# Performance work log

Measured on AMD Instinct MI355X. Metric: run time of the kernel, lower is better.

The kernel has to match this reference:

```python
import jax, jax.numpy as jnp
import numpy as np
from jax import lax

D = 256      # key/query dim
D_F = 256    # diff feature channels
C_TOK = 1    # leading context tokens in query_vit
EPS = 1e-6


def conv2d(x, w, b, pad):
    out = lax.conv_general_dilated(x, w, (1, 1), [(pad, pad), (pad, pad)],
                                   dimension_numbers=('NCHW', 'OIHW', 'NCHW'))
    return out + b[None, :, None, None]


def gn1(x, g, b):
    # GroupNorm with 1 group: normalize over (C,H,W) per sample
    mu = jnp.mean(x, axis=(1, 2, 3), keepdims=True)
    var = jnp.var(x, axis=(1, 2, 3), keepdims=True)
    xn = (x - mu) * lax.rsqrt(var + EPS)
    return xn * g[None, :, None, None] + b[None, :, None, None]


def resize_bilinear_ac(x, Ho, Wo):
    # F.interpolate(mode='bilinear', align_corners=True)
    B, C, H, W = x.shape
    ys = jnp.linspace(0.0, H - 1.0, Ho)
    xs = jnp.linspace(0.0, W - 1.0, Wo)
    y0 = jnp.floor(ys).astype(jnp.int32)
    y1 = jnp.minimum(y0 + 1, H - 1)
    wy = (ys - y0)[None, None, :, None]
    x0 = jnp.floor(xs).astype(jnp.int32)
    x1 = jnp.minimum(x0 + 1, W - 1)
    wx = (xs - x0)[None, None, None, :]
    r = x[:, :, y0, :] * (1.0 - wy) + x[:, :, y1, :] * wy
    return r[:, :, :, x0] * (1.0 - wx) + r[:, :, :, x1] * wx


def setup_inputs() -> dict:
    key = jax.random.key(0)
    ks = jax.random.split(key, 12)
    B, Hd, Wd, Ht, Wt = 8, 64, 64, 32, 32

    def kaiming(k, shape, fan_in):
        return jax.random.normal(k, shape, jnp.float32) * np.sqrt(2.0 / fan_in)

    return {
        'query_vit': jax.random.normal(ks[0], (B, C_TOK + Ht * Wt, D), jnp.float32),
        'feat_diff_cat': jax.random.normal(ks[1], (B, 5 * D_F, Hd, Wd), jnp.float32),
        'rb_w1': kaiming(ks[2], (D_F, 5 * D_F, 3, 3), 5 * D_F * 9), 'rb_b1': jnp.zeros((D_F,), jnp.float32),
        'rb_w2': kaiming(ks[3], (D_F, D_F, 3, 3), D_F * 9), 'rb_b2': jnp.zeros((D_F,), jnp.float32),
        'rb_ws': kaiming(ks[4], (D_F, 5 * D_F, 1, 1), 5 * D_F), 'rb_bs': jnp.zeros((D_F,), jnp.float32),
        'ln_g': jnp.ones((D_F,), jnp.float32), 'ln_b': jnp.zeros((D_F,), jnp.float32),
        'key_w': kaiming(ks[5], (D, D_F, 1, 1), D_F), 'key_b': jnp.zeros((D,), jnp.float32),
        'val_w': kaiming(ks[6], (D_F, D_F, 1, 1), D_F), 'val_b': jnp.zeros((D_F,), jnp.float32),
        'dh0_w': kaiming(ks[7], (D_F, D_F, 3, 3), D_F * 9), 'dh0_b': jnp.zeros((D_F,), jnp.float32),
        'dh1_w': kaiming(ks[8], (D_F, D_F, 3, 3), D_F * 9), 'dh1_b': jnp.zeros((D_F,), jnp.float32),
    }


def reference(query_vit, feat_diff_cat, rb_w1, rb_b1, rb_w2, rb_b2, rb_ws, rb_bs,
              ln_g, ln_b, key_w, key_b, val_w, val_b, dh0_w, dh0_b, dh1_w, dh1_b):
    B, _, h_diff, w_diff = feat_diff_cat.shape
    N = query_vit.shape[1] - C_TOK
    h_trm = w_trm = int(N ** 0.5)

    # ResBlock_ysh(D_f*5 -> D_f): conv3x3 + relu + conv3x3, 1x1-projected residual
    h = jax.nn.relu(conv2d(feat_diff_cat, rb_w1, rb_b1, 1))
    h = conv2d(h, rb_w2, rb_b2, 1)
    feat_diff = jax.nn.relu(h + conv2d(feat_diff_cat, rb_ws, rb_bs, 0))

    fln = gn1(feat_diff, ln_g, ln_b)
    key_diff = conv2d(fln, key_w, key_b, 0).reshape(B, D, -1)          # (B, D, HW)
    value_diff = conv2d(fln, val_w, val_b, 0).reshape(B, D_F, -1)      # (B, Df, HW)
    value_diff = jnp.transpose(value_diff, (0, 2, 1))                  # (B, HW, Df)

    # cross attention: (B, C+N, D) @ (B, D, HW) -> softmax -> @ (B, HW, Df)
    scores = jnp.einsum('bnd,bdm->bnm', query_vit, key_diff) * (D ** -0.5)
    attn = jax.nn.softmax(scores, axis=-1)
    out_cross = jnp.einsum('bnm,bmf->bnf', attn, value_diff)           # (B, C+N, Df)

    out_cross_c = out_cross[:, :C_TOK, :]
    out_p = jnp.transpose(out_cross[:, C_TOK:, :], (0, 2, 1)).reshape(B, D_F, h_trm, w_trm)
    out_p = jax.nn.relu(conv2d(out_p, dh0_w, dh0_b, 1))
    out_p = resize_bilinear_ac(out_p, h_diff, w_diff)
    out_p = out_p + feat_diff                                          # DropPath(0) = identity
    out_p = jax.nn.relu(conv2d(gn1(out_p, ln_g, ln_b), dh1_w, dh1_b, 1)) + out_p
    return out_cross_c, out_p
```

## Files before the change

kernel.cpp:

```cpp
#include <hip/hip_runtime.h>
#include <cstdint>
#include <cstddef>

typedef __attribute__((ext_vector_type(4))) float     f32x4;
typedef __attribute__((ext_vector_type(8))) __bf16    bf16x8;
typedef __attribute__((ext_vector_type(8))) short     short8;
typedef __attribute__((ext_vector_type(4))) unsigned short u16x4;
typedef unsigned short u16;

__device__ __forceinline__ float b2f(u16 u) {
  unsigned x = ((unsigned)u) << 16;
  float f;
  __builtin_memcpy(&f, &x, 4);
  return f;
}
__device__ __forceinline__ u16 f2b(float f) {
  unsigned u;
  __builtin_memcpy(&u, &f, 4);
  return (u16)((u + 0x7FFFu + ((u >> 16) & 1u)) >> 16);
}

struct GP {
  const u16*  A;
  const u16*  B;
  const float* bias;
  const void* aux;
  void*       C;
  float*      out0;
  float*      st;
  long long   aBS, bBS, cBS, auxBS, biasBS;
  int Ktot, Mrows, ldc;
  int cin, logW, wpad, poff;
  float scale;
};

#define GLDS16(g, l)                                                        \
  __builtin_amdgcn_global_load_lds(                                         \
      (const void __attribute__((address_space(1)))*)(g),                   \
      (void __attribute__((address_space(3)))*)(l), 16, 0, 0)

struct G256 {
  const u16* A;
  const u16* B;
  float* P;
  long long aBS;
  int Ktot, cin, logW, wpad, poff;
};

__global__ __launch_bounds__(512, 2) void k_gemm256(G256 gp) {
  const int tid = threadIdx.x;
  const int l = tid & 63, w = tid >> 6;
  const int lr = l & 15, lc = l >> 4;
  const int id = blockIdx.x;
  const int xcd = id & 7, slot = id >> 3;
  const int sp = xcd >> 2;
  const int u = (xcd & 3) * 32 + slot;
  const int mt = u & 15;
  const int b = u >> 4;
  const int m0 = mt << 8;
  const int wm = w >> 2, wn = w & 3;

  __shared__ __align__(16) u16 sm[4][16384];
  u16* smb = &sm[0][0];

  f32x4 acc[8][4];
#pragma unroll
  for (int i = 0; i < 8; ++i)
#pragma unroll
    for (int j = 0; j < 4; ++j) acc[i][j] = (f32x4){0.f, 0.f, 0.f, 0.f};

  const u16* Ab = gp.A + (size_t)b * gp.aBS;
  const u16* aS[2];
  const u16* bS[2];
#pragma unroll
  for (int j = 0; j < 2; ++j) {
    const int r = j * 128 + w * 16 + (l >> 2);
    const int p = m0 + r;
    const int y = p >> gp.logW, x = p & ((1 << gp.logW) - 1);
    const int sw = ((l & 3) ^ ((r >> 1) & 3)) << 3;
    aS[j] = Ab + (size_t)((y + gp.poff) * gp.wpad + (x + gp.poff)) * gp.cin + sw;
    bS[j] = gp.B + (size_t)r * gp.Ktot + sw;
  }

  const int NH = gp.Ktot >> 6;
  const int kt0h = sp * NH;
  int off = kt0h << 5;
  int tap = off / gp.cin;
  int kcS = off - tap * gp.cin;
  int dxS = tap % 3;
  int tapS = (tap / 3) * gp.wpad + dxS;
  int hgS = kt0h;

  auto stage = [&](int h) {
    const int hb = h & 3;
    const int kB = hgS << 5;
    const int kA = tapS * gp.cin + kcS;
    kcS += 32;
    if (kcS == gp.cin) {
      kcS = 0; ++dxS; ++tapS;
      if (dxS == 3) { dxS = 0; tapS += gp.wpad - 3; }
    }
    ++hgS;
    u16* base = smb + hb * 16384 + (w * 16) * 32 + l * 8;
    GLDS16(aS[0] + kA, base);
    GLDS16(aS[1] + kA, base + 4096);
    GLDS16(bS[0] + kB, base + 8192);
    GLDS16(bS[1] + kB, base + 12288);
  };

  stage(0);
  stage(1);
  stage(2);
  asm volatile("s_waitcnt vmcnt(8)" ::: "memory");
  __builtin_amdgcn_s_barrier();

  bf16x8 av[8], bv[4];
  {
    const char* b0 = (const char*)smb;
#pragma unroll
    for (int mi = 0; mi < 8; ++mi) {
      const int row = wm * 128 + mi * 16 + lr;
      av[mi] = *(const bf16x8*)(b0 + row * 64 + ((lc ^ ((row >> 1) & 3)) << 4));
    }
#pragma unroll
    for (int ni = 0; ni < 4; ++ni) {
      const int row = wn * 64 + ni * 16 + lr;
      bv[ni] = *(const bf16x8*)(b0 + 16384 + row * 64 +
                                ((lc ^ ((row >> 1) & 3)) << 4));
    }
  }

  for (int h = 0; h < NH; ++h) {
    if (h + 3 < NH) stage(h + 3);
    const int rem = NH - 1 - h;
    if (rem > 0) {
      if (rem > 2)
        asm volatile("s_waitcnt vmcnt(8)" ::: "memory");
      else if (rem == 2)
        asm volatile("s_waitcnt vmcnt(4)" ::: "memory");
      else
        asm volatile("s_waitcnt vmcnt(0)" ::: "memory");
      asm volatile("s_waitcnt lgkmcnt(0)" ::: "memory");
      __builtin_amdgcn_s_barrier();
    }

    const bool pf = (h + 1 < NH);
    const char* nxt = (const char*)smb + ((h + 1) & 3) * 32768;

#pragma unroll
    for (int mi = 0; mi < 8; ++mi) {
      const int row = wm * 128 + mi * 16 + lr;
      const int sw = (lc ^ ((row >> 1) & 3)) << 4;
#pragma unroll
      for (int ni = 0; ni < 4; ++ni)
        acc[mi][ni] = __builtin_amdgcn_mfma_f32_16x16x32_bf16(
            av[mi], bv[ni], acc[mi][ni], 0, 0, 0);
      if (pf) av[mi] = *(const bf16x8*)(nxt + row * 64 + sw);
    }
    if (pf) {
#pragma unroll
      for (int ni = 0; ni < 4; ++ni) {
        const int row = wn * 64 + ni * 16 + lr;
        bv[ni] = *(const bf16x8*)(nxt + 16384 + row * 64 +
                                  ((lc ^ ((row >> 1) & 3)) << 4));
      }
    }
  }

  float* P = gp.P + ((size_t)sp * 128 + b * 16 + mt) * 65536;
#pragma unroll
  for (int mi = 0; mi < 8; ++mi)
#pragma unroll
    for (int ni = 0; ni < 4; ++ni) {
      const int ncol = wn * 64 + ni * 16 + lr;
      const int mloc = wm * 128 + mi * 16 + lc * 4;
#pragma unroll
      for (int r = 0; r < 4; ++r)
        P[(size_t)(mloc + r) * 256 + ncol] = acc[mi][ni][r];
    }
}

__global__ __launch_bounds__(256) void k_reduceH1(const float* __restrict__ P,
                                                  const float* __restrict__ bias,
                                                  u16* __restrict__ o) {
  const int i4 = blockIdx.x * 256 + threadIdx.x;
  const int flat = i4 << 2;
  const int n0 = flat & 255;
  const int mloc = (flat >> 8) & 255;
  const int gm = flat >> 16;
  const f32x4 a = *(const f32x4*)(P + (size_t)gm * 65536 + mloc * 256 + n0);
  const f32x4 c = *(const f32x4*)(P + (size_t)(128 + gm) * 65536 + mloc * 256 + n0);
  const f32x4 bb = *(const f32x4*)(bias + n0);
  const int batch = gm >> 4;
  const int mg = (gm & 15) * 256 + mloc;
  const int y = mg >> 6, x = mg & 63;
  u16x4 r;
#pragma unroll
  for (int k = 0; k < 4; ++k) r[k] = f2b(fmaxf(a[k] + c[k] + bb[k], 0.f));
  *(u16x4*)(o + ((size_t)batch * 4356 + (size_t)(y + 1) * 66 + x + 1) * 256 + n0) = r;
}

template <int AMODE, int CW>
__global__ __launch_bounds__(512, 2) void k_gemm8(GP gp) {
  const int tid = threadIdx.x;
  const int l = tid & 63, w = tid >> 6;
  const int b = blockIdx.z;
  const int m0 = blockIdx.x * 128;
  const int wm = w >> 2, wn = w & 3;
  const int lr = l & 15, lc = l >> 4;

  __shared__ __align__(16) u16 sm[2][24576];

  f32x4 acc[4][4];
#pragma unroll
  for (int i = 0; i < 4; ++i)
#pragma unroll
    for (int j = 0; j < 4; ++j) acc[i][j] = (f32x4){0.f, 0.f, 0.f, 0.f};

  const u16* Ab = gp.A + (size_t)b * gp.aBS;
  const u16* Bb = gp.B + (size_t)b * gp.bBS;
  const int scoff = (((tid & 7) ^ ((tid >> 3) & 7)) << 3);

  const u16* aP[2];
  const u16* aP2[2];
#pragma unroll
  for (int i = 0; i < 2; ++i) {
    const int p = m0 + i * 64 + (tid >> 3);
    const int y = p >> 6, x = p & 63;
    aP[i] = Ab + (size_t)(y * 66 + x) * gp.cin + scoff;
    if (AMODE == 2) {
      const u16* Xb = (const u16*)gp.aux + (size_t)b * gp.auxBS;
      aP2[i] = Xb + (size_t)((y + 1) * 66 + (x + 1)) * 1280 + scoff;
    }
  }
  const u16* bP[4];
#pragma unroll
  for (int i = 0; i < 4; ++i)
    bP[i] = Bb + (size_t)(i * 64 + (tid >> 3)) * gp.Ktot + scoff;

  const int NT = gp.Ktot >> 6;
  const int seg1t = (AMODE == 2) ? 36 : 0x7fffffff;
  int kcS = 0, tapS = 0, dxS = 0, nstg = 0;

  auto stage = [&](int buf) {
    const int kt = nstg++;
    const int kB = kt << 6;
    u16* sA = &sm[buf][0] + (w << 9);
    u16* sB = &sm[buf][8192] + (w << 9);
    if (AMODE == 2 && kt >= seg1t) {
      const int kA = (kt - seg1t) << 6;
      GLDS16(aP2[0] + kA, sA);
      GLDS16(aP2[1] + kA, sA + 4096);
    } else {
      const int kA = tapS * gp.cin + kcS;
      kcS += 64;
      if (kcS == gp.cin) {
        kcS = 0; ++dxS; ++tapS;
        if (dxS == 3) { dxS = 0; tapS += 63; }
      }
      GLDS16(aP[0] + kA, sA);
      GLDS16(aP[1] + kA, sA + 4096);
    }
    GLDS16(bP[0] + kB, sB);
    GLDS16(bP[1] + kB, sB + 4096);
    GLDS16(bP[2] + kB, sB + 8192);
    GLDS16(bP[3] + kB, sB + 12288);
  };

  stage(0);
  asm volatile("s_waitcnt vmcnt(0)" ::: "memory");
  __builtin_amdgcn_s_barrier();

  for (int t = 0; t < NT; ++t) {
    const int buf = t & 1;
    const u16* sAc = &sm[buf][0];
    const u16* sBc = &sm[buf][8192];
    if (t + 1 < NT) stage(buf ^ 1);

    bf16x8 av0[4], av1[4], bv0[4], bv1[4];
#pragma unroll
    for (int mi = 0; mi < 4; ++mi) {
      const int row = wm * 64 + mi * 16 + lr;
      av0[mi] = *(const bf16x8*)(sAc + row * 64 + (((0 + lc) ^ (row & 7)) << 3));
      av1[mi] = *(const bf16x8*)(sAc + row * 64 + (((4 + lc) ^ (row & 7)) << 3));
    }
#pragma unroll
    for (int ni = 0; ni < 4; ++ni) {
      const int row = wn * 64 + ni * 16 + lr;
      bv0[ni] = *(const bf16x8*)(sBc + row * 64 + (((0 + lc) ^ (row & 7)) << 3));
      bv1[ni] = *(const bf16x8*)(sBc + row * 64 + (((4 + lc) ^ (row & 7)) << 3));
    }
#pragma unroll
    for (int mi = 0; mi < 4; ++mi)
#pragma unroll
      for (int ni = 0; ni < 4; ++ni)
        acc[mi][ni] = __builtin_amdgcn_mfma_f32_16x16x32_bf16(
            av0[mi], bv0[ni], acc[mi][ni], 0, 0, 0);
#pragma unroll
    for (int mi = 0; mi < 4; ++mi)
#pragma unroll
      for (int ni = 0; ni < 4; ++ni)
        acc[mi][ni] = __builtin_amdgcn_mfma_f32_16x16x32_bf16(
            av1[mi], bv1[ni], acc[mi][ni], 0, 0, 0);
    asm volatile("s_waitcnt vmcnt(0)" ::: "memory");
    __builtin_amdgcn_s_barrier();
  }

  float lsum = 0.f, lsq = 0.f;
#pragma unroll
  for (int mi = 0; mi < 4; ++mi) {
#pragma unroll
    for (int ni = 0; ni < 4; ++ni) {
      const int ncol = wn * 64 + ni * 16 + lr;
      const int mbase = m0 + wm * 64 + mi * 16 + lc * 4;
      const float bv_ = gp.bias[ncol];
      if constexpr (CW == 8) {
        float* F = (float*)gp.C + (size_t)b * gp.cBS;
        u16* FB = (u16*)gp.out0 + (size_t)b * gp.cBS;
#pragma unroll
        for (int r = 0; r < 4; ++r) {
          float v = fmaxf(acc[mi][ni][r] + bv_, 0.f);
          const size_t idx = (size_t)(mbase + r) * 256 + ncol;
          F[idx] = v;
          FB[idx] = f2b(v);
          lsum += v;
          lsq += v * v;
        }
      } else {
        float* Cf =
            (float*)gp.C + (size_t)b * gp.cBS + (size_t)ncol * 4096 + mbase;
        const float* mid = (const float*)gp.aux + (size_t)b * gp.auxBS;
        f32x4 o;
#pragma unroll
        for (int r = 0; r < 4; ++r) {
          float v = fmaxf(acc[mi][ni][r] + bv_, 0.f);
          o[r] = v + mid[(size_t)(mbase + r) * 256 + ncol];
        }
        *(f32x4*)Cf = o;
      }
    }
  }
  if constexpr (CW == 8) {
    __syncthreads();
#pragma unroll
    for (int o = 32; o; o >>= 1) {
      lsum += __shfl_down(lsum, o);
      lsq += __shfl_down(lsq, o);
    }
    float* red = (float*)&sm[0][0];
    if (l == 0) { red[w * 2] = lsum; red[w * 2 + 1] = lsq; }
    __syncthreads();
    if (tid == 0) {
      float s = 0.f, s2 = 0.f;
#pragma unroll
      for (int k = 0; k < 8; ++k) { s += red[k * 2]; s2 += red[k * 2 + 1]; }
      atomicAdd(&gp.st[b * 2], s);
      atomicAdd(&gp.st[b * 2 + 1], s2);
    }
  }
}

template <int AMODE, int CW, bool RELU>
__global__ __launch_bounds__(256, 2) void k_gemm(GP gp) {
  const int tid = threadIdx.x;
  const int l = tid & 63, w = tid >> 6;
  const int b = blockIdx.z;
  const int m0 = blockIdx.x * 128, n0 = blockIdx.y * 128;
  const int wm = w >> 1, wn = w & 1;

  __shared__ __align__(16) u16 smA[128 * 64];
  __shared__ __align__(16) u16 smB[128 * 64];

  f32x4 acc[4][4];
#pragma unroll
  for (int i = 0; i < 4; ++i)
#pragma unroll
    for (int j = 0; j < 4; ++j) acc[i][j] = (f32x4){0.f, 0.f, 0.f, 0.f};

  const u16* Ab = gp.A + (size_t)b * gp.aBS;
  const u16* Bb = gp.B + (size_t)b * gp.bBS;

  const int scoff = (((l & 7) ^ (l >> 3)) << 3);

  const u16* aRow[4];
  const u16* bRow[4];
  u16* ldsA[4];
  u16* ldsB[4];
#pragma unroll
  for (int i = 0; i < 4; ++i) {
    const int r = w * 32 + i * 8 + (l >> 3);
    bRow[i] = Bb + (size_t)(n0 + r) * gp.Ktot + scoff;
    const int p = m0 + r;
    if (AMODE == 0) {
      const int pc = p < gp.Mrows ? p : gp.Mrows - 1;
      aRow[i] = Ab + (size_t)pc * gp.Ktot + scoff;
    } else {
      const int y = p >> gp.logW, x = p & ((1 << gp.logW) - 1);
      const int icoord = (y + gp.poff) * gp.wpad + (x + gp.poff);
      aRow[i] = Ab + (size_t)icoord * gp.cin + scoff;
    }
    ldsA[i] = smA + (w * 32 + i * 8) * 64;
    ldsB[i] = smB + (w * 32 + i * 8) * 64;
  }

  const int ktiles = gp.Ktot >> 6;
  int tap_off = 0, dx = 0, kc = 0;

  for (int kt = 0; kt < ktiles; ++kt) {
    int koffA;
    if (AMODE == 0)
      koffA = kt << 6;
    else
      koffA = tap_off * gp.cin + kc;
    const int koffB = kt << 6;
#pragma unroll
    for (int i = 0; i < 4; ++i) GLDS16(aRow[i] + koffA, ldsA[i]);
#pragma unroll
    for (int i = 0; i < 4; ++i) GLDS16(bRow[i] + koffB, ldsB[i]);

    if (AMODE == 1) {
      kc += 64;
      if (kc == gp.cin) {
        kc = 0;
        ++dx;
        ++tap_off;
        if (dx == 3) { dx = 0; tap_off += gp.wpad - 3; }
      }
    }

    __syncthreads();
#pragma unroll
    for (int ks = 0; ks < 2; ++ks) {
      bf16x8 av[4], bv[4];
      const int cc = (ks << 2) + (l >> 4);
#pragma unroll
      for (int mi = 0; mi < 4; ++mi) {
        const int row = wm * 64 + mi * 16 + (l & 15);
        av[mi] = *(const bf16x8*)((const char*)smA + (row << 7) +
                                  ((cc ^ (row & 7)) << 4));
      }
#pragma unroll
      for (int ni = 0; ni < 4; ++ni) {
        const int row = wn * 64 + ni * 16 + (l & 15);
        bv[ni] = *(const bf16x8*)((const char*)smB + (row << 7) +
                                  ((cc ^ (row & 7)) << 4));
      }
#pragma unroll
      for (int mi = 0; mi < 4; ++mi)
#pragma unroll
        for (int ni = 0; ni < 4; ++ni)
          acc[mi][ni] = __builtin_amdgcn_mfma_f32_16x16x32_bf16(
              av[mi], bv[ni], acc[mi][ni], 0, 0, 0);
    }
    __syncthreads();
  }

#pragma unroll
  for (int mi = 0; mi < 4; ++mi) {
#pragma unroll
    for (int ni = 0; ni < 4; ++ni) {
      const int ncol = n0 + wn * 64 + ni * 16 + (l & 15);
      const int mbase = m0 + wm * 64 + mi * 16 + ((l >> 4) << 2);
      const float bv_ =
          gp.bias ? gp.bias[(size_t)b * gp.biasBS + ncol] : 0.f;

      if constexpr (CW == 7) {
        u16* base = (u16*)gp.C;
        if (ncol < 256) {
#pragma unroll
          for (int r = 0; r < 4; ++r)
            base[(size_t)b * 1048576 + (size_t)(mbase + r) * 256 + ncol] =
                f2b(acc[mi][ni][r] + bv_);
        } else {
          u16x4 pk;
#pragma unroll
          for (int r = 0; r < 4; ++r) pk[r] = f2b(acc[mi][ni][r] + bv_);
          *(u16x4*)(base + 8388608 + (size_t)b * 1048576 +
                    (size_t)(ncol - 256) * 4096 + mbase) = pk;
        }
      } else {
#pragma unroll
        for (int reg = 0; reg < 4; ++reg) {
          const int mrow = mbase + reg;
          if (mrow >= gp.Mrows) continue;
          float v = acc[mi][ni][reg] * gp.scale + bv_;
          if (RELU) v = v > 0.f ? v : 0.f;
          if constexpr (CW == 0) {
            ((u16*)gp.C)[(size_t)b * gp.cBS + (size_t)mrow * gp.ldc + ncol] =
                f2b(v);
          } else if constexpr (CW == 4) {
            if (mrow == 0) {
              gp.out0[(size_t)b * 256 + ncol] = v;
            } else {
              const int p = mrow - 1, y = p >> 5, x = p & 31;
              ((u16*)gp.C)[(size_t)b * gp.cBS +
                           (size_t)((y + 1) * 34 + (x + 1)) * 256 + ncol] =
                  f2b(v);
            }
          } else if constexpr (CW == 5) {
            ((float*)gp.C)[(size_t)b * gp.cBS + (size_t)mrow * 256 + ncol] = v;
          }
        }
      }
    }
  }
}


__global__ __launch_bounds__(256) void k_prep_x(const float* __restrict__ x,
                                                u16* __restrict__ o) {
  __shared__ float t[32][65];
  const int b = blockIdx.z, c0 = blockIdx.y << 5, y = blockIdx.x;
  const float* src = x + ((size_t)b * 1280 + c0) * 4096 + (size_t)y * 64;
#pragma unroll
  for (int i = 0; i < 8; ++i) {
    const int idx = threadIdx.x + (i << 8);
    const int c = idx >> 6, xx = idx & 63;
    t[c][xx] = src[(size_t)c * 4096 + xx];
  }
  __syncthreads();
  u16* dst = o + ((size_t)b * 4356 + (size_t)(y + 1) * 66 + 1) * 1280 + c0;
  const int xx = threadIdx.x >> 2;
  const int cq = (threadIdx.x & 3) << 3;
  short8 pk;
#pragma unroll
  for (int j = 0; j < 8; ++j) pk[j] = (short)f2b(t[cq + j][xx]);
  *(short8*)(dst + (size_t)xx * 1280 + cq) = pk;
}

__device__ __forceinline__ void zb1(u16* p, int P, int C, int idx) {
  const int per_img = (4 * P - 4) * C;
  const int b = idx / per_img;
  const int r = idx % per_img;
  const int pix = r / C, c = r % C;
  int y, x;
  const int Pm = P - 1;
  if (pix < P) { y = 0; x = pix; }
  else if (pix < 2 * P) { y = Pm; x = pix - P; }
  else if (pix < 3 * P - 2) { y = pix - 2 * P + 1; x = 0; }
  else { y = pix - (3 * P - 2) + 1; x = Pm; }
  p[((size_t)b * P * P + (size_t)y * P + x) * C + c] = 0;
}

__global__ __launch_bounds__(256) void k_zero_borders(u16* XPAD, u16* H1,
                                                      u16* G2, u16* OCP) {
  const int nx = 8 * 260 * 1280;
  const int nh = 8 * 260 * 256;
  const int no = 8 * 132 * 256;
  const int total = nx + 2 * nh + no;
  for (int i = blockIdx.x * 256 + threadIdx.x; i < total;
       i += gridDim.x * 256) {
    if (i < nx) zb1(XPAD, 66, 1280, i);
    else if (i < nx + nh) zb1(H1, 66, 256, i - nx);
    else if (i < nx + 2 * nh) zb1(G2, 66, 256, i - nx - nh);
    else zb1(OCP, 34, 256, i - nx - 2 * nh);
  }
}

__global__ __launch_bounds__(256) void k_prep_all(
    const float* __restrict__ w1, const float* __restrict__ w2,
    const float* __restrict__ wsc, const float* __restrict__ wd0,
    const float* __restrict__ wd1, const float* __restrict__ b2,
    const float* __restrict__ bsc, const float* __restrict__ q,
    u16* __restrict__ W1R, u16* __restrict__ WCAT2, u16* __restrict__ WD0R,
    u16* __restrict__ WD1R, float* __restrict__ BB2, u16* __restrict__ QB) {
  const int N1 = 2949120, N2 = 917504, N3 = 589824, N4 = 589824,
            N5 = 2099200, N6 = 256;
  const int T = N1 + N2 + N3 + N4 + N5 + N6;
  for (int i = blockIdx.x * 256 + threadIdx.x; i < T; i += gridDim.x * 256) {
    if (i < N1) {
      const int ci = i % 1280, r = i / 1280, t = r % 9, co = r / 9;
      W1R[i] = f2b(w1[((size_t)co * 1280 + ci) * 9 + t]);
    } else if (i < N1 + N2) {
      const int k = i - N1;
      const int co = k / 3584, kk = k % 3584;
      float v;
      if (kk < 2304) {
        const int tap = kk / 256, ci = kk % 256;
        v = w2[((size_t)co * 256 + ci) * 9 + tap];
      } else {
        v = wsc[(size_t)co * 1280 + (kk - 2304)];
      }
      WCAT2[k] = f2b(v);
    } else if (i < N1 + N2 + N3) {
      const int k = i - N1 - N2;
      const int ci = k % 256, r = k / 256, t = r % 9, co = r / 9;
      WD0R[k] = f2b(wd0[((size_t)co * 256 + ci) * 9 + t]);
    } else if (i < N1 + N2 + N3 + N4) {
      const int k = i - N1 - N2 - N3;
      const int ci = k % 256, r = k / 256, t = r % 9, co = r / 9;
      WD1R[k] = f2b(wd1[((size_t)co * 256 + ci) * 9 + t]);
    } else if (i < N1 + N2 + N3 + N4 + N5) {
      const int k = i - N1 - N2 - N3 - N4;
      QB[k] = f2b(q[k] * 0.0625f);
    } else {
      const int k = i - N1 - N2 - N3 - N4 - N5;
      BB2[k] = b2[k] + bsc[k];
    }
  }
}

__global__ __launch_bounds__(256) void k_foldkv(
    const float* __restrict__ wk, const float* __restrict__ wv,
    const float* __restrict__ bk, const float* __restrict__ bv,
    const float* __restrict__ g, const float* __restrict__ lnb,
    const float* __restrict__ st, u16* __restrict__ WKVB,
    float* __restrict__ BKVB) {
  const int idx = blockIdx.x * 256 + threadIdx.x;
  const int b = idx >> 9, j = idx & 511;
  const float mu = st[b * 2] * (1.f / 1048576.f);
  const float var = st[b * 2 + 1] * (1.f / 1048576.f) - mu * mu;
  const float rs = rsqrtf(var + 1e-6f);
  const float* wrow = (j < 256) ? wk + (size_t)j * 256 : wv + (size_t)(j - 256) * 256;
  float acc = (j < 256) ? bk[j] : bv[j - 256];
  u16* orow = WKVB + ((size_t)b * 512 + j) * 256;
  for (int c = 0; c < 256; ++c) {
    const float wv_ = wrow[c];
    orow[c] = f2b(wv_ * g[c] * rs);
    acc += wv_ * (lnb[c] - mu * rs * g[c]);
  }
  BKVB[b * 512 + j] = acc;
}

template <bool PAD>
__global__ __launch_bounds__(256) void k_gn_norm(const float* __restrict__ x,
                                                 const float* __restrict__ st,
                                                 const float* __restrict__ g,
                                                 const float* __restrict__ bb,
                                                 u16* __restrict__ o) {
  const int b = blockIdx.y;
  const float mu = st[b * 2] * (1.f / 1048576.f);
  const float var = st[b * 2 + 1] * (1.f / 1048576.f) - mu * mu;
  const float rs = rsqrtf(var + 1e-6f);
  const int i4 = blockIdx.x * 256 + threadIdx.x;
  const f32x4 v = ((const f32x4*)(x + (size_t)b * 1048576))[i4];
  const int flat = i4 << 2;
  const int c = flat & 255;
  const int p = flat >> 8;
  const f32x4 gv = *(const f32x4*)(g + c);
  const f32x4 bv = *(const f32x4*)(bb + c);
  u16x4 r;
#pragma unroll
  for (int k = 0; k < 4; ++k) r[k] = f2b((v[k] - mu) * rs * gv[k] + bv[k]);
  size_t oidx;
  if (PAD) {
    const int y = p >> 6, xx = p & 63;
    oidx = ((size_t)b * 4356 + (size_t)(y + 1) * 66 + xx + 1) * 256 + c;
  } else {
    oidx = ((size_t)b * 4096 + p) * 256 + c;
  }
  *(u16x4*)(o + oidx) = r;
}

__global__ __launch_bounds__(256) void k_softmax(u16* __restrict__ s) {
  const size_t row = blockIdx.x;
  u16* p = s + row * 4096;
  const int t = threadIdx.x;
  const short8 r0 = ((const short8*)p)[t];
  const short8 r1 = ((const short8*)p)[t + 256];
  float v[16];
#pragma unroll
  for (int i = 0; i < 8; ++i) {
    v[i] = b2f((u16)r0[i]);
    v[8 + i] = b2f((u16)r1[i]);
  }
  float m = v[0];
#pragma unroll
  for (int i = 1; i < 16; ++i) m = fmaxf(m, v[i]);
#pragma unroll
  for (int o = 32; o; o >>= 1) m = fmaxf(m, __shfl_xor(m, o));
  __shared__ float lm[4], lsum[4];
  const int w = t >> 6;
  if ((t & 63) == 0) lm[w] = m;
  __syncthreads();
  m = fmaxf(fmaxf(lm[0], lm[1]), fmaxf(lm[2], lm[3]));
  float sum = 0.f;
#pragma unroll
  for (int i = 0; i < 16; ++i) {
    v[i] = __expf(v[i] - m);
    sum += v[i];
  }
#pragma unroll
  for (int o = 32; o; o >>= 1) sum += __shfl_xor(sum, o);
  if ((t & 63) == 0) lsum[w] = sum;
  __syncthreads();
  sum = lsum[0] + lsum[1] + lsum[2] + lsum[3];
  const float inv = 1.f / sum;
  short8 o0, o1;
#pragma unroll
  for (int i = 0; i < 8; ++i) {
    o0[i] = (short)f2b(v[i] * inv);
    o1[i] = (short)f2b(v[8 + i] * inv);
  }
  ((short8*)p)[t] = o0;
  ((short8*)p)[t + 256] = o1;
}

__global__ __launch_bounds__(256) void k_resize_add(const float* __restrict__ d0,
                                                    const float* __restrict__ F,
                                                    float* __restrict__ mid,
                                                    float* __restrict__ st) {
  const int b = blockIdx.y;
  const float* db = d0 + (size_t)b * 262144;
  const float* Fb = F + (size_t)b * 1048576;
  float* mb = mid + (size_t)b * 1048576;
  float ls = 0.f, lq = 0.f;
  for (int i4 = blockIdx.x * 256 + threadIdx.x; i4 < 262144;
       i4 += 64 * 256) {
    const int flat = i4 << 2;
    const int c = flat & 255;
    const int p = flat >> 8;
    const int y = p >> 6, x = p & 63;
    const float fy = y * (31.f / 63.f);
    const int y0 = (int)fy;
    const float wy = fy - y0;
    const int y1 = y0 + 1 > 31 ? 31 : y0 + 1;
    const float fx = x * (31.f / 63.f);
    const int x0 = (int)fx;
    const float wx = fx - x0;
    const int x1 = x0 + 1 > 31 ? 31 : x0 + 1;
    const f32x4 a = *(const f32x4*)(db + ((size_t)(y0 * 32 + x0) << 8) + c);
    const f32x4 bq = *(const f32x4*)(db + ((size_t)(y0 * 32 + x1) << 8) + c);
    const f32x4 cq = *(const f32x4*)(db + ((size_t)(y1 * 32 + x0) << 8) + c);
    const f32x4 dq = *(const f32x4*)(db + ((size_t)(y1 * 32 + x1) << 8) + c);
    f32x4 r = (a * (1.f - wx) + bq * wx) * (1.f - wy) +
              (cq * (1.f - wx) + dq * wx) * wy;
    r += *(const f32x4*)(Fb + flat);
    *(f32x4*)(mb + flat) = r;
    ls += r[0] + r[1] + r[2] + r[3];
    lq += r[0] * r[0] + r[1] * r[1] + r[2] * r[2] + r[3] * r[3];
  }
#pragma unroll
  for (int o = 32; o; o >>= 1) {
    ls += __shfl_down(ls, o);
    lq += __shfl_down(lq, o);
  }
  __shared__ float red[8];
  const int w = threadIdx.x >> 6;
  if ((threadIdx.x & 63) == 0) { red[w * 2] = ls; red[w * 2 + 1] = lq; }
  __syncthreads();
  if (threadIdx.x == 0) {
    atomicAdd(&st[16 + b * 2], red[0] + red[2] + red[4] + red[6]);
    atomicAdd(&st[16 + b * 2 + 1], red[1] + red[3] + red[5] + red[7]);
  }
}


extern "C" void kernel_launch(void* const* d_in, const int* in_sizes, int n_in,
                              void* d_out, int out_size, void* d_ws,
                              size_t ws_size, hipStream_t stream) {
  (void)in_sizes; (void)n_in; (void)out_size;

  const float* q   = (const float*)d_in[0];
  const float* xdc = (const float*)d_in[1];
  const float* w1  = (const float*)d_in[2];
  const float* b1  = (const float*)d_in[3];
  const float* w2  = (const float*)d_in[4];
  const float* b2  = (const float*)d_in[5];
  const float* wsc = (const float*)d_in[6];
  const float* bsc = (const float*)d_in[7];
  const float* lng = (const float*)d_in[8];
  const float* lnb = (const float*)d_in[9];
  const float* wk  = (const float*)d_in[10];
  const float* bk  = (const float*)d_in[11];
  const float* wv  = (const float*)d_in[12];
  const float* bv  = (const float*)d_in[13];
  const float* wd0 = (const float*)d_in[14];
  const float* bd0 = (const float*)d_in[15];
  const float* wd1 = (const float*)d_in[16];
  const float* bd1 = (const float*)d_in[17];

  char* ws = (char*)d_ws;
  size_t cur = 0;
  auto alloc = [&](size_t sz) {
    char* p = ws + cur;
    cur += sz;
    return p;
  };
  u16* XPAD  = (u16*)alloc(89194496);
  u16* W1R   = (u16*)alloc(5898240);
  u16* WCAT2 = (u16*)alloc(1835008);
  u16* WD0R  = (u16*)alloc(1179648);
  u16* WD1R  = (u16*)alloc(1179648);
  u16* WKVB  = (u16*)alloc(2097152);
  float* BKVB = (float*)alloc(16384);
  float* BB2 = (float*)alloc(1024);
  u16* H1    = (u16*)alloc(17842176);
  float* F   = (float*)alloc(33554432);
  u16* FB    = (u16*)alloc(16777216);
  u16* KT    = (u16*)alloc(16777216);
  u16* V     = (u16*)alloc(16777216);
  u16* QB    = (u16*)alloc(4198400);
  u16* OCP   = (u16*)alloc(4734976);
  float* D0O = (float*)alloc(8388608);
  float* MID = (float*)alloc(33554432);
  u16* G2    = (u16*)alloc(17842176);
  float* ST  = (float*)alloc(256);
  u16* SCORES = XPAD;
  float* PART = (float*)F;
  (void)V;

  if (ws_size < cur) return;

  float* out0 = (float*)d_out;
  float* out1 = (float*)d_out + 2048;

  hipMemsetAsync(ST, 0, 256, stream);
  k_zero_borders<<<2048, 256, 0, stream>>>(XPAD, H1, G2, OCP);
  k_prep_x<<<dim3(64, 40, 8), 256, 0, stream>>>(xdc, XPAD);
  k_prep_all<<<4096, 256, 0, stream>>>(w1, w2, wsc, wd0, wd1, b2, bsc, q, W1R,
                                       WCAT2, WD0R, WD1R, BB2, QB);

  {
    G256 g{};
    g.A = XPAD; g.B = W1R; g.P = PART;
    g.aBS = 5575680; g.Ktot = 11520;
    g.cin = 1280; g.logW = 6; g.wpad = 66; g.poff = 0;
    k_gemm256<<<256, 512, 0, stream>>>(g);
    k_reduceH1<<<8192, 256, 0, stream>>>(PART, b1, H1);
  }
  {
    GP g{};
    g.A = H1; g.B = WCAT2; g.bias = BB2; g.aux = XPAD; g.C = F;
    g.out0 = (float*)FB; g.st = ST;
    g.aBS = 1115136; g.bBS = 0; g.cBS = 1048576; g.auxBS = 5575680;
    g.Ktot = 3584; g.Mrows = 4096; g.ldc = 256;
    g.cin = 256; g.logW = 6; g.wpad = 66; g.poff = 0; g.scale = 1.f;
    k_gemm8<2, 8><<<dim3(32, 1, 8), 512, 0, stream>>>(g);
  }
  k_foldkv<<<16, 256, 0, stream>>>(wk, wv, bk, bv, lng, lnb, ST, WKVB, BKVB);
  {
    GP g{};
    g.A = FB; g.B = WKVB; g.bias = BKVB; g.C = KT;
    g.aBS = 1048576; g.bBS = 131072; g.cBS = 0; g.biasBS = 512;
    g.Ktot = 256; g.Mrows = 4096; g.ldc = 256; g.scale = 1.f;
    k_gemm<0, 7, false><<<dim3(32, 4, 8), 256, 0, stream>>>(g);
  }
  {
    GP g{};
    g.A = QB; g.B = KT; g.bias = nullptr; g.C = SCORES;
    g.aBS = 262400; g.bBS = 1048576; g.cBS = 4198400;
    g.Ktot = 256; g.Mrows = 1025; g.ldc = 4096; g.scale = 1.f;
    k_gemm<0, 0, false><<<dim3(9, 32, 8), 256, 0, stream>>>(g);
  }
  k_softmax<<<8200, 256, 0, stream>>>(SCORES);
  {
    GP g{};
    g.A = SCORES; g.B = V; g.bias = nullptr; g.C = OCP; g.out0 = out0;
    g.aBS = 4198400; g.bBS = 1048576; g.cBS = 295936;
    g.Ktot = 4096; g.Mrows = 1025; g.ldc = 256; g.scale = 1.f;
    k_gemm<0, 4, false><<<dim3(9, 2, 8), 256, 0, stream>>>(g);
  }
  {
    GP g{};
    g.A = OCP; g.B = WD0R; g.bias = bd0; g.C = D0O;
    g.aBS = 295936; g.bBS = 0; g.cBS = 262144; g.biasBS = 0;
    g.Ktot = 2304; g.Mrows = 1024; g.ldc = 256;
    g.cin = 256; g.logW = 5; g.wpad = 34; g.poff = 0; g.scale = 1.f;
    k_gemm<1, 5, true><<<dim3(8, 2, 8), 256, 0, stream>>>(g);
  }
  k_resize_add<<<dim3(64, 8), 256, 0, stream>>>(D0O, F, MID, ST);
  k_gn_norm<true><<<dim3(1024, 8), 256, 0, stream>>>(MID, ST + 16, lng, lnb, G2);
  {
    GP g{};
    g.A = G2; g.B = WD1R; g.bias = bd1; g.C = out1; g.aux = MID;
    g.aBS = 1115136; g.bBS = 0; g.cBS = 1048576; g.auxBS = 1048576;
    g.Ktot = 2304; g.Mrows = 4096; g.ldc = 256;
    g.cin = 256; g.logW = 6; g.wpad = 66; g.poff = 0; g.scale = 1.f;
    k_gemm8<1, 6><<<dim3(32, 1, 8), 512, 0, stream>>>(g);
  }
}
```

Measured before the change: 684.1 us.

## Split-K the attention-times-value GEMM into four partitions with a reduction kernel

Replaces the single attention@V GEMM (K=4096, only 144 blocks) with a split-K kernel that partitions K into four chunks, giving four times as many blocks. Each split writes fp32 partial sums into a reused scratch buffer, and a separate reduce kernel sums them and performs the original epilogue (context token to out0, scatter into the padded bf16 OCP buffer). The aim is better GPU occupancy on an under-filled launch, at the cost of extra fp32 partial traffic and one more kernel launch.

```diff
diff --git a/kernel.cpp b/kernel.cpp
--- a/kernel.cpp
+++ b/kernel.cpp
@@ -488,21 +488,126 @@
           if constexpr (CW == 0) {
             ((u16*)gp.C)[(size_t)b * gp.cBS + (size_t)mrow * gp.ldc + ncol] =
                 f2b(v);
-          } else if constexpr (CW == 4) {
-            if (mrow == 0) {
-              gp.out0[(size_t)b * 256 + ncol] = v;
-            } else {
-              const int p = mrow - 1, y = p >> 5, x = p & 31;
-              ((u16*)gp.C)[(size_t)b * gp.cBS +
-                           (size_t)((y + 1) * 34 + (x + 1)) * 256 + ncol] =
-                  f2b(v);
-            }
           } else if constexpr (CW == 5) {
             ((float*)gp.C)[(size_t)b * gp.cBS + (size_t)mrow * 256 + ncol] = v;
           }
         }
       }
     }
+  }
+}
+
+__global__ __launch_bounds__(256, 2) void k_attnv(const u16* __restrict__ S,
+                                                  const u16* __restrict__ Vv,
+                                                  float* __restrict__ PAV) {
+  const int tid = threadIdx.x;
+  const int l = tid & 63, w = tid >> 6;
+  const int b = blockIdx.z >> 2, sp = blockIdx.z & 3;
+  const int m0 = blockIdx.x * 128, n0 = blockIdx.y * 128;
+  const int wm = w >> 1, wn = w & 1;
+
+  __shared__ __align__(16) u16 smA[128 * 64];
+  __shared__ __align__(16) u16 smB[128 * 64];
+
+  f32x4 acc[4][4];
+#pragma unroll
+  for (int i = 0; i < 4; ++i)
+#pragma unroll
+    for (int j = 0; j < 4; ++j) acc[i][j] = (f32x4){0.f, 0.f, 0.f, 0.f};
+
+  const u16* Ab = S + (size_t)b * 4198400 + sp * 1024;
+  const u16* Bb = Vv + (size_t)b * 1048576 + sp * 1024;
+  const int scoff = (((l & 7) ^ (l >> 3)) << 3);
+
+  const u16* aRow[4];
+  const u16* bRow[4];
+  u16* ldsA[4];
+  u16* ldsB[4];
+#pragma unroll
+  for (int i = 0; i < 4; ++i) {
+    const int r = w * 32 + i * 8 + (l >> 3);
+    bRow[i] = Bb + (size_t)(n0 + r) * 4096 + scoff;
+    const int p = m0 + r;
+    const int pc = p < 1025 ? p : 1024;
+    aRow[i] = Ab + (size_t)pc * 4096 + scoff;
+    ldsA[i] = smA + (w * 32 + i * 8) * 64;
+    ldsB[i] = smB + (w * 32 + i * 8) * 64;
+  }
+
+  for (int kt = 0; kt < 16; ++kt) {
+    const int koff = kt << 6;
+#pragma unroll
+    for (int i = 0; i < 4; ++i) GLDS16(aRow[i] + koff, ldsA[i]);
+#pragma unroll
+    for (int i = 0; i < 4; ++i) GLDS16(bRow[i] + koff, ldsB[i]);
+
+    __syncthreads();
+#pragma unroll
+    for (int ks = 0; ks < 2; ++ks) {
+      bf16x8 av[4], bv[4];
+      const int cc = (ks << 2) + (l >> 4);
+#pragma unroll
+      for (int mi = 0; mi < 4; ++mi) {
+        const int row = wm * 64 + mi * 16 + (l & 15);
+        av[mi] = *(const bf16x8*)((const char*)smA + (row << 7) +
+                                  ((cc ^ (row & 7)) << 4));
+      }
+#pragma unroll
+      for (int ni = 0; ni < 4; ++ni) {
+        const int row = wn * 64 + ni * 16 + (l & 15);
+        bv[ni] = *(const bf16x8*)((const char*)smB + (row << 7) +
+                                  ((cc ^ (row & 7)) << 4));
+      }
+#pragma unroll
+      for (int mi = 0; mi < 4; ++mi)
+#pragma unroll
+        for (int ni = 0; ni < 4; ++ni)
+          acc[mi][ni] = __builtin_amdgcn_mfma_f32_16x16x32_bf16(
+              av[mi], bv[ni], acc[mi][ni], 0, 0, 0);
+    }
+    __syncthreads();
+  }
+
+  float* P = PAV + (size_t)blockIdx.z * 262400;
+#pragma unroll
+  for (int mi = 0; mi < 4; ++mi) {
+#pragma unroll
+    for (int ni = 0; ni < 4; ++ni) {
+      const int ncol = n0 + wn * 64 + ni * 16 + (l & 15);
+      const int mbase = m0 + wm * 64 + mi * 16 + ((l >> 4) << 2);
+#pragma unroll
+      for (int r = 0; r < 4; ++r) {
+        const int mrow = mbase + r;
+        if (mrow >= 1025) continue;
+        P[(size_t)mrow * 256 + ncol] = acc[mi][ni][r];
+      }
+    }
+  }
+}
+
+__global__ __launch_bounds__(256) void k_reduceAttn(const float* __restrict__ PAV,
+                                                    float* __restrict__ out0,
+                                                    u16* __restrict__ OCP) {
+  const int b = blockIdx.y;
+  const int i4 = blockIdx.x * 256 + threadIdx.x;
+  if (i4 >= 65600) return;
+  const int flat = i4 << 2;
+  const int row = flat >> 8;
+  const int col = flat & 255;
+  const float* base = PAV + (size_t)(b * 4) * 262400 + (size_t)row * 256 + col;
+  f32x4 s = *(const f32x4*)base;
+  s += *(const f32x4*)(base + 262400);
+  s += *(const f32x4*)(base + 524800);
+  s += *(const f32x4*)(base + 787200);
+  if (row == 0) {
+    *(f32x4*)(out0 + (size_t)b * 256 + col) = s;
+  } else {
+    const int p = row - 1, y = p >> 5, x = p & 31;
+    u16x4 r;
+#pragma unroll
+    for (int k = 0; k < 4; ++k) r[k] = f2b(s[k]);
+    *(u16x4*)(OCP + ((size_t)b * 1156 + (size_t)(y + 1) * 34 + x + 1) * 256 +
+              col) = r;
   }
 }
 
@@ -798,6 +903,7 @@
   float* ST  = (float*)alloc(256);
   u16* SCORES = XPAD;
   float* PART = (float*)F;
+  float* PAV  = D0O;
   (void)V;
 
   if (ws_size < cur) return;
@@ -844,13 +950,8 @@
     k_gemm<0, 0, false><<<dim3(9, 32, 8), 256, 0, stream>>>(g);
   }
   k_softmax<<<8200, 256, 0, stream>>>(SCORES);
-  {
-    GP g{};
-    g.A = SCORES; g.B = V; g.bias = nullptr; g.C = OCP; g.out0 = out0;
-    g.aBS = 4198400; g.bBS = 1048576; g.cBS = 295936;
-    g.Ktot = 4096; g.Mrows = 1025; g.ldc = 256; g.scale = 1.f;
-    k_gemm<0, 4, false><<<dim3(9, 2, 8), 256, 0, stream>>>(g);
-  }
+  k_attnv<<<dim3(9, 2, 32), 256, 0, stream>>>(SCORES, V, PAV);
+  k_reduceAttn<<<dim3(257, 8), 256, 0, stream>>>(PAV, out0, OCP);
   {
     GP g{};
     g.A = OCP; g.B = WD0R; g.bias = bd0; g.C = D0O;
```

Measured after the change: 661.8 us. 1.03x faster.
